# Performance work log

Hardware: AMD Instinct MI355X
Metric: run time of the kernel (lower is better)

## Reference

```python
import jax, jax.numpy as jnp
import numpy as np

B, L, D = 4, 2048, 512
DK = D // 2
DH = 256.0  # scaling denominator


def _skew(QE):
    # QE: [B, L, M] with M == L (relative position logits via skewing trick)
    b, l, m = QE.shape
    pad = jnp.zeros((b, l, 1), QE.dtype)
    cat = jnp.concatenate([pad, QE], axis=2)      # [B, L, M+1]
    reshaped = cat.reshape(b, m + 1, l)           # [B, M+1, L]
    return reshaped[:, 1:, :]                     # [B, M, L]


def setup_inputs() -> dict:
    key = jax.random.key(0)
    ks = jax.random.split(key, 7)
    return {
        "inputQ": jax.random.normal(ks[0], (B, L, D), jnp.float32),
        "inputK": jax.random.normal(ks[1], (B, L, D), jnp.float32),
        "inputV": jax.random.normal(ks[2], (B, L, D), jnp.float32),
        "Wq": jax.random.normal(ks[3], (D, DK), jnp.float32) * 0.02,
        "Wk": jax.random.normal(ks[4], (D, DK), jnp.float32) * 0.02,
        "Wv": jax.random.normal(ks[5], (D, D), jnp.float32) * 0.02,
        "E": jax.random.normal(ks[6], (L, DK), jnp.float32) * 0.02,
    }


def reference(inputQ, inputK, inputV, Wq, Wk, Wv, E):
    Q = jnp.einsum('bld,dk->blk', inputQ, Wq)   # [B, L, DK]
    K = jnp.einsum('bld,dk->blk', inputK, Wk)   # [B, L, DK]
    V = jnp.einsum('bld,de->ble', inputV, Wv)   # [B, L, D]
    QE = jnp.einsum('blk,mk->blm', Q, E)        # [B, L, max_seq]
    Srel = _skew(QE)                             # [B, L, L]
    QKt = jnp.einsum('blk,bmk->blm', Q, K)      # [B, L, L]
    attn = jax.nn.softmax((QKt + Srel) / jnp.sqrt(jnp.float32(DH)), axis=-1)
    return jnp.einsum('blm,bme->ble', attn, V)  # [B, L, D]
```

## Files before the change

kernel.cpp:

```cpp
#include <hip/hip_runtime.h>
#include <hip/hip_bf16.h>

#define BB 4
#define LL 2048
#define DD 512
#define DKK 256

typedef __bf16 bf16;
typedef __bf16 bf16x4 __attribute__((ext_vector_type(4)));
typedef __bf16 bf16x8 __attribute__((ext_vector_type(8)));
typedef float f32x4 __attribute__((ext_vector_type(4)));

__device__ __forceinline__ void async_ld16(const bf16* g, bf16* l) {
    __builtin_amdgcn_global_load_lds(
        (const __attribute__((address_space(1))) void*)g,
        (__attribute__((address_space(3))) void*)l, 16, 0, 0);
}

__global__ void conv3_f32_bf16(const float* __restrict__ a, const float* __restrict__ bq,
                               const float* __restrict__ c,
                               bf16* __restrict__ oa, bf16* __restrict__ ob,
                               bf16* __restrict__ oc, int n4) {
    const float* in = (blockIdx.y == 0) ? a : (blockIdx.y == 1) ? bq : c;
    bf16* out = (blockIdx.y == 0) ? oa : (blockIdx.y == 1) ? ob : oc;
    int i = blockIdx.x * 256 + threadIdx.x;
    if (i < n4) {
        f32x4 v = *(const f32x4*)(in + (size_t)i * 4);
        bf16x4 o;
        #pragma unroll
        for (int j = 0; j < 4; ++j) o[j] = (bf16)v[j];
        *(bf16x4*)(out + (size_t)i * 4) = o;
    }
}

__global__ void conv_f32_bf16v(const float* __restrict__ in, bf16* __restrict__ out, int n4) {
    int i = blockIdx.x * 256 + threadIdx.x;
    if (i < n4) {
        f32x4 v = *(const f32x4*)(in + (size_t)i * 4);
        bf16x4 o;
        #pragma unroll
        for (int j = 0; j < 4; ++j) o[j] = (bf16)v[j];
        *(bf16x4*)(out + (size_t)i * 4) = o;
    }
}

__global__ void transpose_f32_bf16(const float* __restrict__ in, bf16* __restrict__ out,
                                   int R, int C) {
    int idx = blockIdx.x * 256 + threadIdx.x;
    if (idx < R * C) {
        int r = idx / C, c = idx % C;
        out[(size_t)c * R + r] = (bf16)in[idx];
    }
}

template <int SKEW, int TRANSV>
__launch_bounds__(256, 2)
__global__ void gemm128(const bf16* __restrict__ A, const bf16* __restrict__ B,
                        bf16* __restrict__ C, int N, int K,
                        long aStride, long bStride, long cStride)
{
    __shared__ bf16 Als[128 * 32];
    __shared__ bf16 Bls[128 * 32];
    __shared__ bf16 tbuf[TRANSV ? 64 * 136 : 1];

    int tid  = threadIdx.x;
    int lane = tid & 63;
    int wid  = tid >> 6;
    int l15  = lane & 15;
    int quad = lane >> 4;
    int nb = N >> 7;
    int gx = blockIdx.x % nb;
    int gy = blockIdx.x / nb;

    const bf16* Ab = A + (size_t)blockIdx.y * aStride + (size_t)gy * 128 * K;
    const bf16* Bb = B + (size_t)blockIdx.y * bStride + (size_t)gx * 128 * K;

    int rl = lane >> 2;
    int sl = lane & 3;
    int half = wid & 1;
    const bf16* gsrc = (wid < 2) ? Ab : Bb;
    bf16* ldst = (wid < 2) ? Als : Bls;

    const bf16* gptr[4];
    #pragma unroll
    for (int u = 0; u < 4; ++u) {
        int inst = half * 4 + u;
        int row  = inst * 16 + rl;
        int c    = (sl - (row >> 1)) & 3;
        gptr[u] = gsrc + (size_t)row * K + c * 8;
    }

    f32x4 acc[4][4];
    #pragma unroll
    for (int i = 0; i < 4; ++i)
        #pragma unroll
        for (int j = 0; j < 4; ++j) acc[i][j] = 0;

    for (int k0 = 0; k0 < K; k0 += 32) {
        #pragma unroll
        for (int u = 0; u < 4; ++u) {
            async_ld16(gptr[u], ldst + (half * 4 + u) * 512);
            gptr[u] += 32;
        }
        __syncthreads();
        bf16x8 fA[4], fB[4];
        #pragma unroll
        for (int rt = 0; rt < 4; ++rt) {
            int row = (wid & 1) * 64 + rt * 16 + l15;
            int s   = (quad + (row >> 1)) & 3;
            fA[rt] = *(const bf16x8*)&Als[row * 32 + s * 8];
        }
        #pragma unroll
        for (int ct = 0; ct < 4; ++ct) {
            int col = (wid >> 1) * 64 + ct * 16 + l15;
            int s   = (quad + (col >> 1)) & 3;
            fB[ct] = *(const bf16x8*)&Bls[col * 32 + s * 8];
        }
        #pragma unroll
        for (int rt = 0; rt < 4; ++rt)
            #pragma unroll
            for (int ct = 0; ct < 4; ++ct)
                acc[rt][ct] = __builtin_amdgcn_mfma_f32_16x16x32_bf16(
                                  fA[rt], fB[ct], acc[rt][ct], 0, 0, 0);
        __syncthreads();
    }

    bf16* Cb = C + (size_t)blockIdx.y * cStride;
    int m0 = gy * 128 + (wid & 1) * 64;
    int n0 = gx * 128 + (wid >> 1) * 64;
    if (TRANSV) {
        #pragma unroll
        for (int p = 0; p < 2; ++p) {
            if ((wid >> 1) == p) {
                #pragma unroll
                for (int rt = 0; rt < 4; ++rt)
                    #pragma unroll
                    for (int ct = 0; ct < 4; ++ct)
                        #pragma unroll
                        for (int r = 0; r < 4; ++r)
                            tbuf[(ct * 16 + l15) * 136
                                 + (wid & 1) * 64 + rt * 16 + quad * 4 + r]
                                = (bf16)acc[rt][ct][r];
            }
            __syncthreads();
            int row = tid >> 2, c0 = (tid & 3) * 32;
            bf16* dst = C + (size_t)(gx * 128 + p * 64 + row) * (BB * LL)
                          + (size_t)gy * 128 + c0;
            #pragma unroll
            for (int q = 0; q < 4; ++q)
                *(bf16x8*)(dst + q * 8) = *(const bf16x8*)&tbuf[row * 136 + c0 + q * 8];
            __syncthreads();
        }
    } else if (!SKEW) {
        #pragma unroll
        for (int rt = 0; rt < 4; ++rt)
            #pragma unroll
            for (int ct = 0; ct < 4; ++ct)
                #pragma unroll
                for (int r = 0; r < 4; ++r) {
                    int m = m0 + rt * 16 + quad * 4 + r;
                    int n = n0 + ct * 16 + l15;
                    Cb[(size_t)m * N + n] = (bf16)acc[rt][ct][r];
                }
    } else {
        #pragma unroll
        for (int rt = 0; rt < 4; ++rt)
            #pragma unroll
            for (int ct = 0; ct < 4; ++ct)
                #pragma unroll
                for (int r = 0; r < 4; ++r) {
                    int row = m0 + rt * 16 + quad * 4 + r;
                    int c   = n0 + ct * 16 + l15;
                    bool lower = (c >= LL - 1 - row);
                    int dr = lower ? row : row - 1;
                    int dc = lower ? c - (LL - 1 - row) : c + row + 1;
                    if (lower || row >= 1)
                        Cb[(size_t)dr * LL + dc] = (bf16)acc[rt][ct][r];
                }
    }
}

__launch_bounds__(256, 2)
__global__ void attn_kernel(const bf16* __restrict__ Qw, const bf16* __restrict__ Kw,
                            const bf16* __restrict__ Vt, const bf16* __restrict__ Srel,
                            float* __restrict__ out)
{
    __shared__ bf16  Klds[64 * 256];
    __shared__ bf16  Vlds[256 * 64];
    __shared__ float Ss[32][68];
    __shared__ bf16  Ps[32][72];
    __shared__ float mSt[32], lSt[32], aSt[32];

    int tid  = threadIdx.x;
    int lane = tid & 63;
    int wid  = tid >> 6;
    int l15  = lane & 15;
    int quad = lane >> 4;

    int xcd = blockIdx.x & 7;
    int b   = xcd >> 1;
    int dh  = xcd & 1;
    int i0  = (blockIdx.x >> 3) * 32;

    const bf16* Qb = Qw + (size_t)b * LL * DKK;
    const bf16* Kb = Kw + (size_t)b * LL * DKK;
    const bf16* Sb = Srel + (size_t)b * LL * LL;
    const bf16* Vb = Vt + (size_t)(dh * 256) * (BB * LL) + (size_t)b * LL;

    const bf16* kptr[8];
    const bf16* vptr[8];
    #pragma unroll
    for (int u = 0; u < 8; ++u) {
        int inst = wid * 8 + u;
        int j_ = inst * 2 + (lane >> 5);
        int ck = ((lane & 31) - j_) & 31;
        kptr[u] = Kb + (size_t)j_ * DKK + ck * 8;
        int d_ = inst * 8 + (lane >> 3);
        int cv = ((lane & 7) - d_) & 7;
        vptr[u] = Vb + (size_t)d_ * (BB * LL) + cv * 8;
    }

    bf16x8 Qreg[2][8];
    #pragma unroll
    for (int rt = 0; rt < 2; ++rt)
        #pragma unroll
        for (int ks = 0; ks < 8; ++ks)
            Qreg[rt][ks] = *(const bf16x8*)(Qb + (size_t)(i0 + rt * 16 + l15) * DKK
                                            + ks * 32 + quad * 8);

    if (tid < 32) { mSt[tid] = -1e30f; lSt[tid] = 0.f; }

    f32x4 accO[2][4];
    #pragma unroll
    for (int rt = 0; rt < 2; ++rt)
        #pragma unroll
        for (int nt = 0; nt < 4; ++nt) accO[rt][nt] = 0;

    asm volatile("s_waitcnt vmcnt(0)" ::: "memory");

    #pragma unroll
    for (int u = 0; u < 8; ++u) {
        async_ld16(kptr[u], Klds + (wid * 8 + u) * 512);
        kptr[u] += 64 * DKK;
    }
    __builtin_amdgcn_sched_barrier(0);
    int srow = i0 + (tid >> 3), ssg = tid & 7;
    bf16x8 srelCur = *(const bf16x8*)(Sb + (size_t)srow * LL + ssg * 8);
    const bf16* sPtr = Sb + (size_t)srow * LL + ssg * 8 + 64;
    __builtin_amdgcn_sched_barrier(0);
    #pragma unroll
    for (int u = 0; u < 8; ++u) {
        async_ld16(vptr[u], Vlds + (wid * 8 + u) * 512);
        vptr[u] += 64;
    }

    int jrow = wid * 16 + l15;

    for (int j0 = 0; j0 < LL; j0 += 64) {
        bool notlast = (j0 + 64 < LL);

        asm volatile("s_waitcnt vmcnt(9)" ::: "memory");
        bf16x8 kf[8];
        #pragma unroll
        for (int ks = 0; ks < 8; ++ks) {
            int cp = (ks * 4 + quad + jrow) & 31;
            kf[ks] = *(const bf16x8*)&Klds[jrow * 256 + cp * 8];
        }
        asm volatile("s_waitcnt lgkmcnt(0)" ::: "memory");
        __builtin_amdgcn_sched_barrier(0);
        if (notlast) {
            #pragma unroll
            for (int u = 0; u < 8; ++u) {
                async_ld16(kptr[u], Klds + (wid * 8 + u) * 512);
                kptr[u] += 64 * DKK;
            }
        }
        __builtin_amdgcn_sched_barrier(0);
        bf16x8 srelNext;
        if (notlast) {
            srelNext = *(const bf16x8*)sPtr;
            sPtr += 64;
        }
        __builtin_amdgcn_sched_barrier(0);
        f32x4 s0 = 0, s1 = 0;
        __builtin_amdgcn_s_setprio(1);
        #pragma unroll
        for (int ks = 0; ks < 8; ++ks) {
            s0 = __builtin_amdgcn_mfma_f32_16x16x32_bf16(Qreg[0][ks], kf[ks], s0, 0, 0, 0);
            s1 = __builtin_amdgcn_mfma_f32_16x16x32_bf16(Qreg[1][ks], kf[ks], s1, 0, 0, 0);
        }
        __builtin_amdgcn_s_setprio(0);
        #pragma unroll
        for (int r = 0; r < 4; ++r) {
            Ss[quad * 4 + r][wid * 16 + l15]      = s0[r];
            Ss[16 + quad * 4 + r][wid * 16 + l15] = s1[r];
        }
        asm volatile("s_waitcnt lgkmcnt(0)\ns_barrier" ::: "memory");

        {
            int r = tid >> 3, sg = tid & 7;
            int i = i0 + r;
            float v[8];
            #pragma unroll
            for (int c = 0; c < 8; ++c) {
                float sr = (j0 + sg * 8 + c == i + 1) ? 0.f : (float)srelCur[c];
                v[c] = (Ss[r][sg * 8 + c] + sr) * 0.0625f;
            }
            float tmax = v[0];
            #pragma unroll
            for (int c = 1; c < 8; ++c) tmax = fmaxf(tmax, v[c]);
            tmax = fmaxf(tmax, __shfl_xor(tmax, 1));
            tmax = fmaxf(tmax, __shfl_xor(tmax, 2));
            tmax = fmaxf(tmax, __shfl_xor(tmax, 4));
            float mOld = mSt[r], lOld = lSt[r];
            float mNew = fmaxf(mOld, tmax);
            float alpha = __expf(mOld - mNew);
            float ps = 0.f;
            bf16x8 pv;
            #pragma unroll
            for (int c = 0; c < 8; ++c) {
                float p = __expf(v[c] - mNew);
                ps += p;
                pv[c] = (bf16)p;
            }
            ps += __shfl_xor(ps, 1);
            ps += __shfl_xor(ps, 2);
            ps += __shfl_xor(ps, 4);
            *(bf16x8*)&Ps[r][sg * 8] = pv;
            if (sg == 0) { mSt[r] = mNew; lSt[r] = alpha * lOld + ps; aSt[r] = alpha; }
        }
        srelCur = srelNext;
        asm volatile("s_waitcnt lgkmcnt(0)\ns_barrier" ::: "memory");

        if (notlast) asm volatile("s_waitcnt vmcnt(9)" ::: "memory");
        else         asm volatile("s_waitcnt vmcnt(0)" ::: "memory");
        bf16x8 aF[2][2];
        #pragma unroll
        for (int rt = 0; rt < 2; ++rt)
            #pragma unroll
            for (int kk = 0; kk < 2; ++kk)
                aF[rt][kk] = *(const bf16x8*)&Ps[rt * 16 + l15][kk * 32 + quad * 8];
        float ar[2][4];
        #pragma unroll
        for (int rt = 0; rt < 2; ++rt)
            #pragma unroll
            for (int r = 0; r < 4; ++r) ar[rt][r] = aSt[rt * 16 + quad * 4 + r];
        bf16x8 vf[4][2];
        #pragma unroll
        for (int nt = 0; nt < 4; ++nt) {
            int dd = wid * 64 + nt * 16 + l15;
            int c0 = (quad + dd) & 7;
            int c1 = (4 + quad + dd) & 7;
            vf[nt][0] = *(const bf16x8*)&Vlds[dd * 64 + c0 * 8];
            vf[nt][1] = *(const bf16x8*)&Vlds[dd * 64 + c1 * 8];
        }
        asm volatile("s_waitcnt lgkmcnt(0)" ::: "memory");
        __builtin_amdgcn_sched_barrier(0);
        if (notlast) {
            #pragma unroll
            for (int u = 0; u < 8; ++u) {
                async_ld16(vptr[u], Vlds + (wid * 8 + u) * 512);
                vptr[u] += 64;
            }
        }
        __builtin_amdgcn_sched_barrier(0);
        __builtin_amdgcn_s_setprio(1);
        #pragma unroll
        for (int nt = 0; nt < 4; ++nt) {
            #pragma unroll
            for (int rt = 0; rt < 2; ++rt) {
                f32x4 o = accO[rt][nt];
                o[0] *= ar[rt][0]; o[1] *= ar[rt][1];
                o[2] *= ar[rt][2]; o[3] *= ar[rt][3];
                o = __builtin_amdgcn_mfma_f32_16x16x32_bf16(aF[rt][0], vf[nt][0], o, 0, 0, 0);
                o = __builtin_amdgcn_mfma_f32_16x16x32_bf16(aF[rt][1], vf[nt][1], o, 0, 0, 0);
                accO[rt][nt] = o;
            }
        }
        __builtin_amdgcn_s_setprio(0);
    }
    float lr[2][4];
    #pragma unroll
    for (int rt = 0; rt < 2; ++rt)
        #pragma unroll
        for (int r = 0; r < 4; ++r) lr[rt][r] = 1.f / lSt[rt * 16 + quad * 4 + r];
    #pragma unroll
    for (int rt = 0; rt < 2; ++rt)
        #pragma unroll
        for (int nt = 0; nt < 4; ++nt)
            #pragma unroll
            for (int r = 0; r < 4; ++r) {
                int i = i0 + rt * 16 + quad * 4 + r;
                int d = dh * 256 + wid * 64 + nt * 16 + l15;
                out[((size_t)b * LL + i) * DD + d] = accO[rt][nt][r] * lr[rt][r];
            }
}

extern "C" void kernel_launch(void* const* d_in, const int* in_sizes, int n_in,
                              void* d_out, int out_size, void* d_ws, size_t ws_size,
                              hipStream_t stream) {
    const float* inQ = (const float*)d_in[0];
    const float* inK = (const float*)d_in[1];
    const float* inV = (const float*)d_in[2];
    const float* Wq  = (const float*)d_in[3];
    const float* Wk  = (const float*)d_in[4];
    const float* Wv  = (const float*)d_in[5];
    const float* E   = (const float*)d_in[6];
    float* out = (float*)d_out;

    char* ws = (char*)d_ws;
    bf16* Qw   = (bf16*)(ws);
    bf16* Kw   = (bf16*)(ws + ((size_t)4  << 20));
    bf16* Vt   = (bf16*)(ws + ((size_t)8  << 20));
    bf16* SrelW= (bf16*)(ws + ((size_t)16 << 20));
    bf16* Xq   = (bf16*)(ws + ((size_t)16 << 20));
    bf16* Xk   = (bf16*)(ws + ((size_t)24 << 20));
    bf16* Xv   = (bf16*)(ws + ((size_t)32 << 20));
    bf16* WqT  = (bf16*)(ws + ((size_t)48 << 20));
    bf16* WkT  = (bf16*)(ws + ((size_t)48 << 20) + 262144);
    bf16* WvT  = (bf16*)(ws + ((size_t)48 << 20) + 524288);
    bf16* Eb   = (bf16*)(ws + ((size_t)49 << 20));

    conv3_f32_bf16<<<dim3(4096, 3), 256, 0, stream>>>(inQ, inK, inV, Xq, Xk, Xv,
                                                      (BB * LL * DD) / 4);
    conv_f32_bf16v<<<512,  256, 0, stream>>>(E, Eb, (LL * DKK) / 4);
    transpose_f32_bf16<<<512,  256, 0, stream>>>(Wq, WqT, DD, DKK);
    transpose_f32_bf16<<<512,  256, 0, stream>>>(Wk, WkT, DD, DKK);
    transpose_f32_bf16<<<1024, 256, 0, stream>>>(Wv, WvT, DD, DD);

    gemm128<0, 0><<<dim3(2 * 64, 2),  256, 0, stream>>>(Xq, WqT, Qw, DKK, DD,
                                                        4194304L, 131072L, 2097152L);
    gemm128<0, 1><<<dim3(4 * 64, 1),  256, 0, stream>>>(Xv, WvT, Vt, DD, DD, 0, 0, 0);
    gemm128<1, 0><<<dim3(16 * 16, BB), 256, 0, stream>>>(Qw, Eb, SrelW, LL, DKK,
                                                         (long)LL * DKK, 0, (long)LL * LL);
    attn_kernel<<<dim3(BB * 64 * 2), 256, 0, stream>>>(Qw, Kw, Vt, SrelW, out);
}
```

Baseline: 235.1 us.

## Compute attention softmax in MFMA registers and merge weight-prep kernels

The attention kernel no longer stages QK scores through an fp32 shared-memory tile for a separate softmax pass. It swaps the MFMA operands so each lane holds a column-oriented score fragment, computes row maxima with shuffles plus a small cross-wave max table, and keeps running max and sum in registers. The Srel tile is now double-buffered in LDS, and its global load is issued earlier. The four small conversion and transpose launches are also merged into one kernel. This removes an LDS round trip and some per-row sequential work, and cuts launch overhead, at the cost of extra barriers and shared-memory exchanges for the partial maxima and sums.

```diff
diff --git a/kernel.cpp b/kernel.cpp
--- a/kernel.cpp
+++ b/kernel.cpp
@@ -33,23 +33,26 @@
     }
 }
 
-__global__ void conv_f32_bf16v(const float* __restrict__ in, bf16* __restrict__ out, int n4) {
-    int i = blockIdx.x * 256 + threadIdx.x;
-    if (i < n4) {
-        f32x4 v = *(const f32x4*)(in + (size_t)i * 4);
-        bf16x4 o;
-        #pragma unroll
-        for (int j = 0; j < 4; ++j) o[j] = (bf16)v[j];
-        *(bf16x4*)(out + (size_t)i * 4) = o;
-    }
-}
-
-__global__ void transpose_f32_bf16(const float* __restrict__ in, bf16* __restrict__ out,
-                                   int R, int C) {
+__global__ void prep_misc(const float* __restrict__ E, const float* __restrict__ Wq,
+                          const float* __restrict__ Wk, const float* __restrict__ Wv,
+                          bf16* __restrict__ Eb, bf16* __restrict__ WqT,
+                          bf16* __restrict__ WkT, bf16* __restrict__ WvT) {
+    int y = blockIdx.y;
     int idx = blockIdx.x * 256 + threadIdx.x;
-    if (idx < R * C) {
-        int r = idx / C, c = idx % C;
-        out[(size_t)c * R + r] = (bf16)in[idx];
+    if (y == 0) {
+        if (idx < (LL * DKK) / 4) {
+            f32x4 v = *(const f32x4*)(E + (size_t)idx * 4);
+            bf16x4 o;
+            #pragma unroll
+            for (int j = 0; j < 4; ++j) o[j] = (bf16)v[j];
+            *(bf16x4*)(Eb + (size_t)idx * 4) = o;
+        }
+    } else if (y == 1) {
+        if (idx < DD * DKK) { int r = idx / DKK, c = idx % DKK; WqT[(size_t)c * DD + r] = (bf16)Wq[idx]; }
+    } else if (y == 2) {
+        if (idx < DD * DKK) { int r = idx / DKK, c = idx % DKK; WkT[(size_t)c * DD + r] = (bf16)Wk[idx]; }
+    } else {
+        if (idx < DD * DD)  { int r = idx / DD,  c = idx % DD;  WvT[(size_t)c * DD + r] = (bf16)Wv[idx]; }
     }
 }
 
@@ -187,9 +190,10 @@
 {
     __shared__ bf16  Klds[64 * 256];
     __shared__ bf16  Vlds[256 * 64];
-    __shared__ float Ss[32][68];
+    __shared__ bf16  SrelL[2][32 * 72];
     __shared__ bf16  Ps[32][72];
-    __shared__ float mSt[32], lSt[32], aSt[32];
+    __shared__ float pmax[32][4];
+    __shared__ float aSt[32];
 
     int tid  = threadIdx.x;
     int lane = tid & 63;
@@ -228,38 +232,41 @@
             Qreg[rt][ks] = *(const bf16x8*)(Qb + (size_t)(i0 + rt * 16 + l15) * DKK
                                             + ks * 32 + quad * 8);
 
-    if (tid < 32) { mSt[tid] = -1e30f; lSt[tid] = 0.f; }
-
     f32x4 accO[2][4];
     #pragma unroll
     for (int rt = 0; rt < 2; ++rt)
         #pragma unroll
         for (int nt = 0; nt < 4; ++nt) accO[rt][nt] = 0;
 
-    asm volatile("s_waitcnt vmcnt(0)" ::: "memory");
-
+    float mreg0 = -1e30f, mreg1 = -1e30f;
+    float lreg0 = 0.f, lreg1 = 0.f;
+
+    int srow = i0 + (tid >> 3), ssg = tid & 7;
+    bf16x8 srelNext = *(const bf16x8*)(Sb + (size_t)srow * LL + ssg * 8);
+    const bf16* sPtr = Sb + (size_t)srow * LL + ssg * 8 + 64;
+    __builtin_amdgcn_sched_barrier(0);
     #pragma unroll
     for (int u = 0; u < 8; ++u) {
         async_ld16(kptr[u], Klds + (wid * 8 + u) * 512);
         kptr[u] += 64 * DKK;
     }
     __builtin_amdgcn_sched_barrier(0);
-    int srow = i0 + (tid >> 3), ssg = tid & 7;
-    bf16x8 srelCur = *(const bf16x8*)(Sb + (size_t)srow * LL + ssg * 8);
-    const bf16* sPtr = Sb + (size_t)srow * LL + ssg * 8 + 64;
-    __builtin_amdgcn_sched_barrier(0);
     #pragma unroll
     for (int u = 0; u < 8; ++u) {
         async_ld16(vptr[u], Vlds + (wid * 8 + u) * 512);
         vptr[u] += 64;
     }
+    __builtin_amdgcn_sched_barrier(0);
+    *(bf16x8*)&SrelL[0][(tid >> 3) * 72 + (tid & 7) * 8] = srelNext;
+    asm volatile("s_waitcnt lgkmcnt(0)\ns_barrier" ::: "memory");
 
     int jrow = wid * 16 + l15;
 
     for (int j0 = 0; j0 < LL; j0 += 64) {
         bool notlast = (j0 + 64 < LL);
-
-        asm volatile("s_waitcnt vmcnt(9)" ::: "memory");
+        int p = (j0 >> 6) & 1;
+
+        asm volatile("s_waitcnt vmcnt(8)" ::: "memory");
         bf16x8 kf[8];
         #pragma unroll
         for (int ks = 0; ks < 8; ++ks) {
@@ -267,6 +274,11 @@
             kf[ks] = *(const bf16x8*)&Klds[jrow * 256 + cp * 8];
         }
         asm volatile("s_waitcnt lgkmcnt(0)" ::: "memory");
+        __builtin_amdgcn_sched_barrier(0);
+        if (notlast) {
+            srelNext = *(const bf16x8*)sPtr;
+            sPtr += 64;
+        }
         __builtin_amdgcn_sched_barrier(0);
         if (notlast) {
             #pragma unroll
@@ -276,63 +288,59 @@
             }
         }
         __builtin_amdgcn_sched_barrier(0);
-        bf16x8 srelNext;
-        if (notlast) {
-            srelNext = *(const bf16x8*)sPtr;
-            sPtr += 64;
-        }
-        __builtin_amdgcn_sched_barrier(0);
+
         f32x4 s0 = 0, s1 = 0;
         __builtin_amdgcn_s_setprio(1);
         #pragma unroll
         for (int ks = 0; ks < 8; ++ks) {
-            s0 = __builtin_amdgcn_mfma_f32_16x16x32_bf16(Qreg[0][ks], kf[ks], s0, 0, 0, 0);
-            s1 = __builtin_amdgcn_mfma_f32_16x16x32_bf16(Qreg[1][ks], kf[ks], s1, 0, 0, 0);
+            s0 = __builtin_amdgcn_mfma_f32_16x16x32_bf16(kf[ks], Qreg[0][ks], s0, 0, 0, 0);
+            s1 = __builtin_amdgcn_mfma_f32_16x16x32_bf16(kf[ks], Qreg[1][ks], s1, 0, 0, 0);
         }
         __builtin_amdgcn_s_setprio(0);
+
+        bf16x4 sr0 = *(const bf16x4*)&SrelL[p][l15 * 72 + wid * 16 + quad * 4];
+        bf16x4 sr1 = *(const bf16x4*)&SrelL[p][(16 + l15) * 72 + wid * 16 + quad * 4];
+        int jb = j0 + wid * 16 + quad * 4;
+        float v0[4], v1[4];
         #pragma unroll
         for (int r = 0; r < 4; ++r) {
-            Ss[quad * 4 + r][wid * 16 + l15]      = s0[r];
-            Ss[16 + quad * 4 + r][wid * 16 + l15] = s1[r];
-        }
+            float a0 = (jb + r == i0 + l15 + 1)      ? 0.f : (float)sr0[r];
+            float a1 = (jb + r == i0 + 16 + l15 + 1) ? 0.f : (float)sr1[r];
+            v0[r] = (s0[r] + a0) * 0.0625f;
+            v1[r] = (s1[r] + a1) * 0.0625f;
+        }
+        float m0 = fmaxf(fmaxf(v0[0], v0[1]), fmaxf(v0[2], v0[3]));
+        float m1 = fmaxf(fmaxf(v1[0], v1[1]), fmaxf(v1[2], v1[3]));
+        m0 = fmaxf(m0, __shfl_xor(m0, 16)); m0 = fmaxf(m0, __shfl_xor(m0, 32));
+        m1 = fmaxf(m1, __shfl_xor(m1, 16)); m1 = fmaxf(m1, __shfl_xor(m1, 32));
+        if (quad == 0) { pmax[l15][wid] = m0; pmax[16 + l15][wid] = m1; }
         asm volatile("s_waitcnt lgkmcnt(0)\ns_barrier" ::: "memory");
 
-        {
-            int r = tid >> 3, sg = tid & 7;
-            int i = i0 + r;
-            float v[8];
-            #pragma unroll
-            for (int c = 0; c < 8; ++c) {
-                float sr = (j0 + sg * 8 + c == i + 1) ? 0.f : (float)srelCur[c];
-                v[c] = (Ss[r][sg * 8 + c] + sr) * 0.0625f;
-            }
-            float tmax = v[0];
-            #pragma unroll
-            for (int c = 1; c < 8; ++c) tmax = fmaxf(tmax, v[c]);
-            tmax = fmaxf(tmax, __shfl_xor(tmax, 1));
-            tmax = fmaxf(tmax, __shfl_xor(tmax, 2));
-            tmax = fmaxf(tmax, __shfl_xor(tmax, 4));
-            float mOld = mSt[r], lOld = lSt[r];
-            float mNew = fmaxf(mOld, tmax);
-            float alpha = __expf(mOld - mNew);
-            float ps = 0.f;
-            bf16x8 pv;
-            #pragma unroll
-            for (int c = 0; c < 8; ++c) {
-                float p = __expf(v[c] - mNew);
-                ps += p;
-                pv[c] = (bf16)p;
-            }
-            ps += __shfl_xor(ps, 1);
-            ps += __shfl_xor(ps, 2);
-            ps += __shfl_xor(ps, 4);
-            *(bf16x8*)&Ps[r][sg * 8] = pv;
-            if (sg == 0) { mSt[r] = mNew; lSt[r] = alpha * lOld + ps; aSt[r] = alpha; }
-        }
-        srelCur = srelNext;
+        f32x4 pm0 = *(const f32x4*)&pmax[l15][0];
+        f32x4 pm1 = *(const f32x4*)&pmax[16 + l15][0];
+        float mf0 = fmaxf(fmaxf(fmaxf(pm0[0], pm0[1]), fmaxf(pm0[2], pm0[3])), mreg0);
+        float mf1 = fmaxf(fmaxf(fmaxf(pm1[0], pm1[1]), fmaxf(pm1[2], pm1[3])), mreg1);
+        float al0 = __expf(mreg0 - mf0); mreg0 = mf0;
+        float al1 = __expf(mreg1 - mf1); mreg1 = mf1;
+        if (notlast)
+            *(bf16x8*)&SrelL[p ^ 1][(tid >> 3) * 72 + (tid & 7) * 8] = srelNext;
+        float ps0 = 0.f, ps1 = 0.f;
+        bf16x4 pv0, pv1;
+        #pragma unroll
+        for (int r = 0; r < 4; ++r) {
+            float e0 = __expf(v0[r] - mf0); ps0 += e0; pv0[r] = (bf16)e0;
+            float e1 = __expf(v1[r] - mf1); ps1 += e1; pv1[r] = (bf16)e1;
+        }
+        ps0 += __shfl_xor(ps0, 16); ps0 += __shfl_xor(ps0, 32);
+        ps1 += __shfl_xor(ps1, 16); ps1 += __shfl_xor(ps1, 32);
+        lreg0 = al0 * lreg0 + ps0;
+        lreg1 = al1 * lreg1 + ps1;
+        *(bf16x4*)&Ps[l15][wid * 16 + quad * 4]      = pv0;
+        *(bf16x4*)&Ps[16 + l15][wid * 16 + quad * 4] = pv1;
+        if (wid == 0 && quad == 0) { aSt[l15] = al0; aSt[16 + l15] = al1; }
         asm volatile("s_waitcnt lgkmcnt(0)\ns_barrier" ::: "memory");
 
-        if (notlast) asm volatile("s_waitcnt vmcnt(9)" ::: "memory");
+        if (notlast) asm volatile("s_waitcnt vmcnt(8)" ::: "memory");
         else         asm volatile("s_waitcnt vmcnt(0)" ::: "memory");
         bf16x8 aF[2][2];
         #pragma unroll
@@ -379,11 +387,17 @@
         }
         __builtin_amdgcn_s_setprio(0);
     }
+
+    if (quad == 0) { pmax[l15][wid] = lreg0; pmax[16 + l15][wid] = lreg1; }
+    asm volatile("s_waitcnt lgkmcnt(0)\ns_barrier" ::: "memory");
     float lr[2][4];
     #pragma unroll
     for (int rt = 0; rt < 2; ++rt)
         #pragma unroll
-        for (int r = 0; r < 4; ++r) lr[rt][r] = 1.f / lSt[rt * 16 + quad * 4 + r];
+        for (int r = 0; r < 4; ++r) {
+            f32x4 lp = *(const f32x4*)&pmax[rt * 16 + quad * 4 + r][0];
+            lr[rt][r] = 1.f / (lp[0] + lp[1] + lp[2] + lp[3]);
+        }
     #pragma unroll
     for (int rt = 0; rt < 2; ++rt)
         #pragma unroll
@@ -423,10 +437,7 @@
 
     conv3_f32_bf16<<<dim3(4096, 3), 256, 0, stream>>>(inQ, inK, inV, Xq, Xk, Xv,
                                                       (BB * LL * DD) / 4);
-    conv_f32_bf16v<<<512,  256, 0, stream>>>(E, Eb, (LL * DKK) / 4);
-    transpose_f32_bf16<<<512,  256, 0, stream>>>(Wq, WqT, DD, DKK);
-    transpose_f32_bf16<<<512,  256, 0, stream>>>(Wk, WkT, DD, DKK);
-    transpose_f32_bf16<<<1024, 256, 0, stream>>>(Wv, WvT, DD, DD);
+    prep_misc<<<dim3(1024, 4), 256, 0, stream>>>(E, Wq, Wk, Wv, Eb, WqT, WkT, WvT);
 
     gemm128<0, 0><<<dim3(2 * 64, 2),  256, 0, stream>>>(Xq, WqT, Qw, DKK, DD,
                                                         4194304L, 131072L, 2097152L);
```

New measurement: 234.7 us. No clear change (-0.2%).
